# Optimization experiments

Measured on AMD Instinct MI355X. Metric: run time of the kernel, lower is better.

The kernel has to match this reference:

```python
import jax, jax.numpy as jnp
import numpy as np
from jax import lax

B, CIN, COUT, K = 4, 128, 128, 3
Z = X = Y = 32
EPS = 1e-8


def setup_inputs() -> dict:
    key = jax.random.key(0)
    k1, k2, k3 = jax.random.split(key, 3)
    x = jax.random.normal(k1, (B, CIN, Z, X, Y), dtype=jnp.float32)
    S = jax.random.normal(k2, (B, CIN), dtype=jnp.float32)
    weight = jax.random.normal(k3, (COUT, CIN, K, K, K), dtype=jnp.float32)
    return {"x": x, "S": S, "weight": weight}


def reference(x, S, weight):
    b, cin, z, xx, yy = x.shape
    cout = weight.shape[0]
    # Per-sample modulated weight: [B, cout, cin, k, k, k]
    W = weight[None] * (S[:, None, :, None, None, None] + 1.0)
    # Demodulation: L2-normalize each (b, cout) filter
    d = lax.rsqrt(jnp.sum(W * W, axis=(2, 3, 4, 5), keepdims=True) + EPS)
    W = W * d
    # Grouped conv3d with groups=B (stride=1, dilation=1 -> same padding = (k-1)//2)
    pad = (K - 1) // 2
    xr = x.reshape(1, b * cin, z, xx, yy)
    Wr = W.reshape(b * cout, cin, K, K, K)
    out = lax.conv_general_dilated(
        xr, Wr,
        window_strides=(1, 1, 1),
        padding=[(pad, pad)] * 3,
        feature_group_count=b,
        dimension_numbers=("NCDHW", "OIDHW", "NCDHW"),
    )
    return out.reshape(b, cout, z, xx, yy)
```

## Files before the change

### kernel.cpp

```cpp
#include <hip/hip_runtime.h>

#define B_    4
#define CIN_  128
#define COUT_ 128
#define EPSF  1e-8f

typedef short  short8  __attribute__((ext_vector_type(8)));
typedef unsigned short ushort8 __attribute__((ext_vector_type(8)));
typedef float  f32x16  __attribute__((ext_vector_type(16)));

#define GLOAD_LDS16(g, l) __builtin_amdgcn_global_load_lds( \
    (const __attribute__((address_space(1))) unsigned int*)(g), \
    (__attribute__((address_space(3))) unsigned int*)(l), 16, 0, 0)

__device__ __forceinline__ unsigned short f2bf(float f) {
    union { float f; unsigned int u; } v; v.f = f;
    unsigned int r = (v.u + 0x7fffu + ((v.u >> 16) & 1u)) >> 16;
    return (unsigned short)r;
}

__global__ __launch_bounds__(128) void scale_kernel(const float* __restrict__ S,
                                                    const float* __restrict__ w,
                                                    float* __restrict__ d) {
    const int co = blockIdx.x;
    const int ci = threadIdx.x;
    const float* wp = w + ((size_t)co * CIN_ + ci) * 27;
    float wsq = 0.f;
#pragma unroll
    for (int k = 0; k < 27; ++k) { float v = wp[k]; wsq += v * v; }
    __shared__ float red[128];
    for (int b = 0; b < B_; ++b) {
        float s = S[b * CIN_ + ci] + 1.0f;
        red[ci] = s * s * wsq;
        __syncthreads();
        for (int off = 64; off > 0; off >>= 1) {
            if (ci < off) red[ci] += red[ci + off];
            __syncthreads();
        }
        if (ci == 0) d[b * COUT_ + co] = rsqrtf(red[0] + EPSF);
        __syncthreads();
    }
}

__global__ __launch_bounds__(256) void wt_kernel(const float* __restrict__ w,
                                                 unsigned short* __restrict__ wtf) {
    int idx = blockIdx.x * 256 + threadIdx.x;
    int e  = idx & 7;
    int l  = (idx >> 3) & 63;
    int c  = (idx >> 9) & 7;
    int ct = (idx >> 12) & 3;
    int ko = idx >> 14;
    int co = ct * 32 + (l & 31);
    int ci = c * 16 + (l >> 5) * 8 + e;
    wtf[idx] = f2bf(w[((size_t)co * CIN_ + ci) * 27 + ko]);
}

__global__ __launch_bounds__(256) void xt_kernel(const float* __restrict__ x,
                                                 const float* __restrict__ S,
                                                 unsigned short* __restrict__ xT) {
    __shared__ float ls[128 * 33];
    const int xx = blockIdx.x, z = blockIdx.y, b = blockIdx.z;
    const int tid = threadIdx.x;
    const size_t base = (size_t)b * 4194304 + (size_t)z * 1024 + xx * 32;
#pragma unroll
    for (int it = 0; it < 4; ++it) {
        int i = tid + it * 256;
        int ci = i >> 3, y4 = (i & 7) * 4;
        float4 v = *(const float4*)(x + base + (size_t)ci * 32768 + y4);
        float s = S[b * CIN_ + ci] + 1.0f;
        ls[ci * 33 + y4 + 0] = v.x * s;
        ls[ci * 33 + y4 + 1] = v.y * s;
        ls[ci * 33 + y4 + 2] = v.z * s;
        ls[ci * 33 + y4 + 3] = v.w * s;
    }
    __syncthreads();
    const size_t obase = (size_t)((b * 32 + z) * 32 + xx) * 4096;
#pragma unroll
    for (int it = 0; it < 2; ++it) {
        int i = tid + it * 256;
        int y = i >> 4, c = (i >> 1) & 7, h = i & 1;
        ushort8 v;
#pragma unroll
        for (int j = 0; j < 8; ++j) v[j] = f2bf(ls[(c * 16 + h * 8 + j) * 33 + y]);
        *(ushort8*)(xT + obase + c * 512 + y * 16 + h * 8) = v;
    }
}

__global__ __launch_bounds__(256, 2) void conv_mfma(const unsigned short* __restrict__ xT,
                                                    const unsigned short* __restrict__ wtf,
                                                    const float* __restrict__ dscale,
                                                    const char* __restrict__ zpage,
                                                    float* __restrict__ out) {
    __shared__ char smem[2][26112];
    const int tid  = threadIdx.x;
    const int lane = tid & 63;
    const int wv   = tid >> 6;
    const int z0 = (blockIdx.x >> 4) * 4;
    const int x0 = (blockIdx.x & 15) * 2;
    const int b  = blockIdx.y;

    const char* xTb = (const char*)xT;
    const char* gsrc[7];
#pragma unroll
    for (int s = 0; s < 7; ++s) {
        int g = tid + s * 256;
        int row = g / 68, rem = g - row * 68;
        int h = rem / 34, yi = rem - h * 34;
        int zg = z0 + (row >> 2) - 1;
        int xg = x0 + (row & 3) - 1;
        bool ok = ((unsigned)zg < 32u) && ((unsigned)xg < 32u) && (yi >= 1) && (yi <= 32);
        gsrc[s] = ok ? (xTb + ((((b * 32 + zg) * 32 + xg) * 8192) + (yi - 1) * 32 + h * 16))
                     : zpage;
    }

    const int bperlane = ((lane >> 5) * 34 + (lane & 31)) * 16;
    const int aperlane = lane * 16;
    const char* wtb = (const char*)wtf;

    f32x16 acc[4][2];
#pragma unroll
    for (int cz = 0; cz < 4; ++cz)
#pragma unroll
        for (int cx = 0; cx < 2; ++cx)
#pragma unroll
            for (int r = 0; r < 16; ++r) acc[cz][cx][r] = 0.f;

#pragma unroll
    for (int s = 0; s < 6; ++s)
        GLOAD_LDS16(gsrc[s], &smem[0][tid * 16 + s * 4096]);
    if (tid < 96)
        GLOAD_LDS16(gsrc[6], &smem[0][tid * 16 + 6 * 4096]);
    __syncthreads();

    for (int c = 0; c < 8; ++c) {
        if (c < 7) {
            const int nb = (c + 1) & 1;
            const int coff = (c + 1) * 1024;
#pragma unroll
            for (int s = 0; s < 6; ++s)
                GLOAD_LDS16(gsrc[s] + coff, &smem[nb][tid * 16 + s * 4096]);
            if (tid < 96)
                GLOAD_LDS16(gsrc[6] + coff, &smem[nb][tid * 16 + 6 * 4096]);
        }
        const char* buf   = smem[c & 1];
        const char* abase = wtb + c * 1024 + wv * 8192;
#pragma unroll
        for (int ky = 0; ky < 3; ++ky) {
            short8 a[9];
#pragma unroll
            for (int t = 0; t < 9; ++t)
                a[t] = *(const short8*)(abase + (t * 3 + ky) * 32768 + aperlane);
            short8 bf[2][4];
#pragma unroll
            for (int xr = 0; xr < 4; ++xr)
                bf[0][xr] = *(const short8*)(buf + (xr * 68 + ky) * 16 + bperlane);
#pragma unroll
            for (int zr = 0; zr < 6; ++zr) {
                if (zr < 5) {
#pragma unroll
                    for (int xr = 0; xr < 4; ++xr)
                        bf[(zr + 1) & 1][xr] = *(const short8*)(buf +
                            (((zr + 1) * 4 + xr) * 68 + ky) * 16 + bperlane);
                }
                __builtin_amdgcn_s_setprio(1);
#pragma unroll
                for (int cz = 0; cz < 4; ++cz) {
                    const int kz = zr - cz;
                    if (kz >= 0 && kz <= 2) {
#pragma unroll
                        for (int cx = 0; cx < 2; ++cx)
#pragma unroll
                        for (int kx = 0; kx < 3; ++kx)
                            acc[cz][cx] = __builtin_amdgcn_mfma_f32_32x32x16_bf16(
                                a[kz * 3 + kx], bf[zr & 1][cx + kx], acc[cz][cx], 0, 0, 0);
                    }
                }
                __builtin_amdgcn_s_setprio(0);
            }
        }
        __syncthreads();
    }

    float dd[16];
#pragma unroll
    for (int r = 0; r < 16; ++r)
        dd[r] = dscale[b * COUT_ + wv * 32 + (r & 3) + 8 * (r >> 2) + 4 * (lane >> 5)];
#pragma unroll
    for (int cz = 0; cz < 4; ++cz)
#pragma unroll
    for (int cx = 0; cx < 2; ++cx) {
        size_t ob = (((size_t)(b * COUT_ + wv * 32) * 32 + (z0 + cz)) * 32 + (x0 + cx)) * 32 + (lane & 31);
#pragma unroll
        for (int r = 0; r < 16; ++r) {
            int row = (r & 3) + 8 * (r >> 2) + 4 * (lane >> 5);
            out[ob + (size_t)row * 32768] = acc[cz][cx][r] * dd[r];
        }
    }
}

__global__ __launch_bounds__(256, 4) void conv_kernel(const float* __restrict__ x,
                                                      const float* __restrict__ S,
                                                      const float* __restrict__ w,
                                                      const float* __restrict__ dscale,
                                                      float* __restrict__ out) {
    __shared__ float xs[6][6][36];
    __shared__ float wsm[27][16];
    const int tid = threadIdx.x;
    const int zt  = blockIdx.x >> 3;
    const int xt  = blockIdx.x & 7;
    const int co0 = blockIdx.y * 16;
    const int b   = blockIdx.z;
    const int z0 = zt * 4, x0 = xt * 4;
    const int lane = tid & 63;
    const int cg = tid >> 6;
    const int zz = (lane >> 4) & 3;
    const int xx = (lane >> 2) & 3;
    const int y0 = (lane & 3) * 8;
    float acc[4][8];
#pragma unroll
    for (int c = 0; c < 4; ++c)
#pragma unroll
        for (int j = 0; j < 8; ++j) acc[c][j] = 0.f;
    for (int ci = 0; ci < CIN_; ++ci) {
        __syncthreads();
        const float* xb = x + (size_t)(b * CIN_ + ci) * 32768;
        const float smod = S[b * CIN_ + ci] + 1.0f;
#pragma unroll
        for (int t = 0; t < 5; ++t) {
            int i = tid + t * 256;
            if (i < 6 * 6 * 34) {
                int zi = i / 204, r = i - zi * 204, xi = r / 34, yi = r - xi * 34;
                int z = z0 + zi - 1, xc = x0 + xi - 1, y = yi - 1;
                float v = 0.f;
                if ((unsigned)z < 32u && (unsigned)xc < 32u && (unsigned)y < 32u)
                    v = xb[z * 1024 + xc * 32 + y] * smod;
                xs[zi][xi][yi] = v;
            }
        }
#pragma unroll
        for (int t = 0; t < 2; ++t) {
            int i = tid + t * 256;
            if (i < 16 * 27) {
                int cog = i / 27, k = i - cog * 27;
                wsm[k][cog] = w[((size_t)(co0 + cog) * CIN_ + ci) * 27 + k];
            }
        }
        __syncthreads();
#pragma unroll
        for (int kz = 0; kz < 3; ++kz)
#pragma unroll
        for (int kx = 0; kx < 3; ++kx) {
            const float* xrow = &xs[zz + kz][xx + kx][y0];
            float xw[10];
#pragma unroll
            for (int q = 0; q < 10; ++q) xw[q] = xrow[q];
            const int kb = (kz * 3 + kx) * 3;
#pragma unroll
            for (int ky = 0; ky < 3; ++ky) {
                float4 wvv = *(const float4*)&wsm[kb + ky][cg * 4];
#pragma unroll
                for (int j = 0; j < 8; ++j) {
                    acc[0][j] = fmaf(xw[ky + j], wvv.x, acc[0][j]);
                    acc[1][j] = fmaf(xw[ky + j], wvv.y, acc[1][j]);
                    acc[2][j] = fmaf(xw[ky + j], wvv.z, acc[2][j]);
                    acc[3][j] = fmaf(xw[ky + j], wvv.w, acc[3][j]);
                }
            }
        }
    }
#pragma unroll
    for (int c = 0; c < 4; ++c) {
        const int co = co0 + cg * 4 + c;
        const float dd = dscale[b * COUT_ + co];
        float* ob = out + (((size_t)(b * COUT_ + co) * 32 + (z0 + zz)) * 32 + (x0 + xx)) * 32 + y0;
#pragma unroll
        for (int j = 0; j < 8; ++j) ob[j] = acc[c][j] * dd;
    }
}

extern "C" void kernel_launch(void* const* d_in, const int* in_sizes, int n_in,
                              void* d_out, int out_size, void* d_ws, size_t ws_size,
                              hipStream_t stream) {
    const float* x = (const float*)d_in[0];
    const float* S = (const float*)d_in[1];
    const float* w = (const float*)d_in[2];
    float* out = (float*)d_out;

    const size_t NEED = 1048576 + 33554432;
    if (ws_size >= NEED) {
        float* dscale = (float*)d_ws;
        char*  zpage  = (char*)d_ws + 4096;
        unsigned short* wtf = (unsigned short*)((char*)d_ws + 12288);
        unsigned short* xT  = (unsigned short*)((char*)d_ws + 1048576);
        hipMemsetAsync(zpage, 0, 8192, stream);
        scale_kernel<<<dim3(COUT_), dim3(128), 0, stream>>>(S, w, dscale);
        wt_kernel<<<dim3(1728), dim3(256), 0, stream>>>(w, wtf);
        xt_kernel<<<dim3(32, 32, 4), dim3(256), 0, stream>>>(x, S, xT);
        conv_mfma<<<dim3(128, 4), dim3(256), 0, stream>>>(xT, wtf, dscale, zpage, out);
    } else {
        float* dscale = (float*)d_ws;
        scale_kernel<<<dim3(COUT_), dim3(128), 0, stream>>>(S, w, dscale);
        conv_kernel<<<dim3(64, 8, 4), dim3(256), 0, stream>>>(x, S, w, dscale, out);
    }
}
```

Before: 121.3 us.

## Split conv_mfma z-rows across 8 waves with 512-thread blocks

The MFMA conv block grows from 4 to 8 waves. Each wave now computes two of the four z output rows for its 32-channel output group, which halves the accumulators per wave and lets more waves be resident. The inner loop is restructured to load A fragments per kz and B fragments per (kz, cz) directly, dropping the double-buffered B register pipeline and the s_setprio hints. In exchange, A fragments are loaded twice per block (once by each z-half wave) and each wave does less reuse of the loaded B rows.

Result: slower. 141.0 us (+16.3%).

```diff
diff --git a/kernel.cpp b/kernel.cpp
--- a/kernel.cpp
+++ b/kernel.cpp
@@ -86,7 +86,7 @@
     }
 }
 
-__global__ __launch_bounds__(256, 2) void conv_mfma(const unsigned short* __restrict__ xT,
+__global__ __launch_bounds__(512, 4) void conv_mfma(const unsigned short* __restrict__ xT,
                                                     const unsigned short* __restrict__ wtf,
                                                     const float* __restrict__ dscale,
                                                     const char* __restrict__ zpage,
@@ -95,15 +95,17 @@
     const int tid  = threadIdx.x;
     const int lane = tid & 63;
     const int wv   = tid >> 6;
+    const int cog  = wv & 3;
+    const int sh   = wv >> 2;
     const int z0 = (blockIdx.x >> 4) * 4;
     const int x0 = (blockIdx.x & 15) * 2;
     const int b  = blockIdx.y;
 
     const char* xTb = (const char*)xT;
-    const char* gsrc[7];
-#pragma unroll
-    for (int s = 0; s < 7; ++s) {
-        int g = tid + s * 256;
+    const char* gsrc[4];
+#pragma unroll
+    for (int s = 0; s < 4; ++s) {
+        int g = tid + s * 512;
         int row = g / 68, rem = g - row * 68;
         int h = rem / 34, yi = rem - h * 34;
         int zg = z0 + (row >> 2) - 1;
@@ -117,19 +119,19 @@
     const int aperlane = lane * 16;
     const char* wtb = (const char*)wtf;
 
-    f32x16 acc[4][2];
-#pragma unroll
-    for (int cz = 0; cz < 4; ++cz)
+    f32x16 acc[2][2];
+#pragma unroll
+    for (int cz = 0; cz < 2; ++cz)
 #pragma unroll
         for (int cx = 0; cx < 2; ++cx)
 #pragma unroll
             for (int r = 0; r < 16; ++r) acc[cz][cx][r] = 0.f;
 
 #pragma unroll
-    for (int s = 0; s < 6; ++s)
-        GLOAD_LDS16(gsrc[s], &smem[0][tid * 16 + s * 4096]);
+    for (int s = 0; s < 3; ++s)
+        GLOAD_LDS16(gsrc[s], &smem[0][tid * 16 + s * 8192]);
     if (tid < 96)
-        GLOAD_LDS16(gsrc[6], &smem[0][tid * 16 + 6 * 4096]);
+        GLOAD_LDS16(gsrc[3], &smem[0][tid * 16 + 3 * 8192]);
     __syncthreads();
 
     for (int c = 0; c < 8; ++c) {
@@ -137,45 +139,34 @@
             const int nb = (c + 1) & 1;
             const int coff = (c + 1) * 1024;
 #pragma unroll
-            for (int s = 0; s < 6; ++s)
-                GLOAD_LDS16(gsrc[s] + coff, &smem[nb][tid * 16 + s * 4096]);
+            for (int s = 0; s < 3; ++s)
+                GLOAD_LDS16(gsrc[s] + coff, &smem[nb][tid * 16 + s * 8192]);
             if (tid < 96)
-                GLOAD_LDS16(gsrc[6] + coff, &smem[nb][tid * 16 + 6 * 4096]);
+                GLOAD_LDS16(gsrc[3] + coff, &smem[nb][tid * 16 + 3 * 8192]);
         }
         const char* buf   = smem[c & 1];
-        const char* abase = wtb + c * 1024 + wv * 8192;
+        const char* abase = wtb + c * 1024 + cog * 8192;
 #pragma unroll
         for (int ky = 0; ky < 3; ++ky) {
-            short8 a[9];
-#pragma unroll
-            for (int t = 0; t < 9; ++t)
-                a[t] = *(const short8*)(abase + (t * 3 + ky) * 32768 + aperlane);
-            short8 bf[2][4];
-#pragma unroll
-            for (int xr = 0; xr < 4; ++xr)
-                bf[0][xr] = *(const short8*)(buf + (xr * 68 + ky) * 16 + bperlane);
-#pragma unroll
-            for (int zr = 0; zr < 6; ++zr) {
-                if (zr < 5) {
-#pragma unroll
-                    for (int xr = 0; xr < 4; ++xr)
-                        bf[(zr + 1) & 1][xr] = *(const short8*)(buf +
-                            (((zr + 1) * 4 + xr) * 68 + ky) * 16 + bperlane);
+#pragma unroll
+            for (int kz = 0; kz < 3; ++kz) {
+                short8 a0 = *(const short8*)(abase + (kz * 9 + 0 + ky) * 32768 + aperlane);
+                short8 a1 = *(const short8*)(abase + (kz * 9 + 3 + ky) * 32768 + aperlane);
+                short8 a2 = *(const short8*)(abase + (kz * 9 + 6 + ky) * 32768 + aperlane);
+#pragma unroll
+                for (int cz = 0; cz < 2; ++cz) {
+                    const char* rbase = buf + (sh * 2 + kz + cz) * 4352 + ky * 16 + bperlane;
+                    short8 b0 = *(const short8*)(rbase);
+                    short8 b1 = *(const short8*)(rbase + 1088);
+                    short8 b2 = *(const short8*)(rbase + 2176);
+                    short8 b3 = *(const short8*)(rbase + 3264);
+                    acc[cz][0] = __builtin_amdgcn_mfma_f32_32x32x16_bf16(a0, b0, acc[cz][0], 0, 0, 0);
+                    acc[cz][1] = __builtin_amdgcn_mfma_f32_32x32x16_bf16(a0, b1, acc[cz][1], 0, 0, 0);
+                    acc[cz][0] = __builtin_amdgcn_mfma_f32_32x32x16_bf16(a1, b1, acc[cz][0], 0, 0, 0);
+                    acc[cz][1] = __builtin_amdgcn_mfma_f32_32x32x16_bf16(a1, b2, acc[cz][1], 0, 0, 0);
+                    acc[cz][0] = __builtin_amdgcn_mfma_f32_32x32x16_bf16(a2, b2, acc[cz][0], 0, 0, 0);
+                    acc[cz][1] = __builtin_amdgcn_mfma_f32_32x32x16_bf16(a2, b3, acc[cz][1], 0, 0, 0);
                 }
-                __builtin_amdgcn_s_setprio(1);
-#pragma unroll
-                for (int cz = 0; cz < 4; ++cz) {
-                    const int kz = zr - cz;
-                    if (kz >= 0 && kz <= 2) {
-#pragma unroll
-                        for (int cx = 0; cx < 2; ++cx)
-#pragma unroll
-                        for (int kx = 0; kx < 3; ++kx)
-                            acc[cz][cx] = __builtin_amdgcn_mfma_f32_32x32x16_bf16(
-                                a[kz * 3 + kx], bf[zr & 1][cx + kx], acc[cz][cx], 0, 0, 0);
-                    }
-                }
-                __builtin_amdgcn_s_setprio(0);
             }
         }
         __syncthreads();
@@ -184,12 +175,13 @@
     float dd[16];
 #pragma unroll
     for (int r = 0; r < 16; ++r)
-        dd[r] = dscale[b * COUT_ + wv * 32 + (r & 3) + 8 * (r >> 2) + 4 * (lane >> 5)];
-#pragma unroll
-    for (int cz = 0; cz < 4; ++cz)
+        dd[r] = dscale[b * COUT_ + cog * 32 + (r & 3) + 8 * (r >> 2) + 4 * (lane >> 5)];
+#pragma unroll
+    for (int cz = 0; cz < 2; ++cz)
 #pragma unroll
     for (int cx = 0; cx < 2; ++cx) {
-        size_t ob = (((size_t)(b * COUT_ + wv * 32) * 32 + (z0 + cz)) * 32 + (x0 + cx)) * 32 + (lane & 31);
+        const int zg = z0 + sh * 2 + cz;
+        size_t ob = (((size_t)(b * COUT_ + cog * 32) * 32 + zg) * 32 + (x0 + cx)) * 32 + (lane & 31);
 #pragma unroll
         for (int r = 0; r < 16; ++r) {
             int row = (r & 3) + 8 * (r >> 2) + 4 * (lane >> 5);
@@ -241,8 +233,8 @@
         for (int t = 0; t < 2; ++t) {
             int i = tid + t * 256;
             if (i < 16 * 27) {
-                int cog = i / 27, k = i - cog * 27;
-                wsm[k][cog] = w[((size_t)(co0 + cog) * CIN_ + ci) * 27 + k];
+                int cog2 = i / 27, k = i - cog2 * 27;
+                wsm[k][cog2] = w[((size_t)(co0 + cog2) * CIN_ + ci) * 27 + k];
             }
         }
         __syncthreads();
@@ -296,7 +288,7 @@
         scale_kernel<<<dim3(COUT_), dim3(128), 0, stream>>>(S, w, dscale);
         wt_kernel<<<dim3(1728), dim3(256), 0, stream>>>(w, wtf);
         xt_kernel<<<dim3(32, 32, 4), dim3(256), 0, stream>>>(x, S, xT);
-        conv_mfma<<<dim3(128, 4), dim3(256), 0, stream>>>(xT, wtf, dscale, zpage, out);
+        conv_mfma<<<dim3(128, 4), dim3(512), 0, stream>>>(xT, wtf, dscale, zpage, out);
     } else {
         float* dscale = (float*)d_ws;
         scale_kernel<<<dim3(COUT_), dim3(128), 0, stream>>>(S, w, dscale);
```
